# Performance work log

Measured on AMD Instinct MI355X. Metric: run time of the kernel, lower is better.

## Reference

```python
import jax, jax.numpy as jnp
import numpy as np

D = 32       # hidden_size (hardcoded in AR.__init__)
H = 16       # num_heads
HD = D // H  # head_dim = 2
L = 8        # num DiT blocks
MLP = 128    # mlp_ratio 4.0
B, S, T, P = 16, 1024, 256, 32
SCALE = float(1.0 / np.sqrt(HD))


def _ln(x, g, b, eps=1e-6):
    mu = jnp.mean(x, axis=-1, keepdims=True)
    var = jnp.mean((x - mu) ** 2, axis=-1, keepdims=True)
    return (x - mu) * jax.lax.rsqrt(var + eps) * g + b


def _mha(q_in, kv_in, in_w, in_b, out_w, out_b):
    # nn.MultiheadAttention math, batch-first layout (permutation-equivalent)
    wq, wk, wv = in_w[:D], in_w[D:2 * D], in_w[2 * D:]
    bq, bk, bv = in_b[:D], in_b[D:2 * D], in_b[2 * D:]
    Bq, Sq = q_in.shape[0], q_in.shape[1]
    Sk = kv_in.shape[1]
    q = (q_in @ wq.T + bq).reshape(Bq, Sq, H, HD)
    k = (kv_in @ wk.T + bk).reshape(Bq, Sk, H, HD)
    v = (kv_in @ wv.T + bv).reshape(Bq, Sk, H, HD)
    scores = jnp.einsum('bqhd,bkhd->bhqk', q, k) * SCALE
    a = jax.nn.softmax(scores, axis=-1)
    o = jnp.einsum('bhqk,bkhd->bqhd', a, v).reshape(Bq, Sq, D)
    return o @ out_w.T + out_b


def setup_inputs() -> dict:
    key = jax.random.key(0)
    ks = iter(jax.random.split(key, 40))
    rn = lambda k, sh, sc=1.0: jax.random.normal(k, sh, jnp.float32) * sc
    inp = {
        'x': rn(next(ks), (B, S, D)),
        'speaker_emb': rn(next(ks), (B, P, D)),
        'text_phonemes': rn(next(ks), (B, T, D)),
        'timestep_emb': rn(next(ks), (B, D)),
        'mask': jnp.ones((S,), jnp.float32),
        # per-block params, stacked over L for lax.scan
        'ln1_g': jnp.ones((L, D)), 'ln1_b': jnp.zeros((L, D)),
        'ln2_g': jnp.ones((L, D)), 'ln2_b': jnp.zeros((L, D)),
        'ln22_g': jnp.ones((L, D)), 'ln22_b': jnp.zeros((L, D)),
        'ln3_g': jnp.ones((L, D)), 'ln3_b': jnp.zeros((L, D)),
        'attn_in_w': rn(next(ks), (L, 3 * D, D), 0.1), 'attn_in_b': jnp.zeros((L, 3 * D)),
        'attn_out_w': rn(next(ks), (L, D, D), 0.1), 'attn_out_b': jnp.zeros((L, D)),
        'cross_in_w': rn(next(ks), (L, 3 * D, D), 0.1), 'cross_in_b': jnp.zeros((L, 3 * D)),
        'cross_out_w': rn(next(ks), (L, D, D), 0.1), 'cross_out_b': jnp.zeros((L, D)),
        'ts_w': rn(next(ks), (L, 2 * D, D), 0.1), 'ts_b': jnp.zeros((L, 2 * D)),
        'fc1_w': rn(next(ks), (L, MLP, D), 0.1), 'fc1_b': jnp.zeros((L, MLP)),
        'fc2_w': rn(next(ks), (L, D, MLP), 0.1), 'fc2_b': jnp.zeros((L, D)),
    }
    return inp


def _forward(x, speaker_emb, text_phonemes, timestep_emb, mask, params):
    m = mask[None, :, None]  # (1, S, 1), matches mask.unsqueeze(0).unsqueeze(2)
    def body(h, p):
        h = h * m
        hn = _ln(h, p['ln1_g'], p['ln1_b'])
        h = h + _mha(hn, hn, p['attn_in_w'], p['attn_in_b'], p['attn_out_w'], p['attn_out_b'])
        # both cross attentions use cross_attn weights (cross_attn2 is dead code in source)
        ca1 = _mha(_ln(h, p['ln2_g'], p['ln2_b']), text_phonemes,
                   p['cross_in_w'], p['cross_in_b'], p['cross_out_w'], p['cross_out_b'])
        ca2 = _mha(_ln(h, p['ln22_g'], p['ln22_b']), speaker_emb,
                   p['cross_in_w'], p['cross_in_b'], p['cross_out_w'], p['cross_out_b'])
        h = h + ca1 + ca2
        ss = timestep_emb @ p['ts_w'].T + p['ts_b']        # (B, 2D)
        scale, shift = ss[:, :D], ss[:, D:]
        hm = _ln(h, p['ln3_g'], p['ln3_b']) * (1.0 + scale[:, None, :]) + shift[:, None, :]
        mlp = jax.nn.gelu(hm @ p['fc1_w'].T + p['fc1_b'], approximate=False) @ p['fc2_w'].T + p['fc2_b']
        return (h + mlp) * m, None
    out, _ = jax.lax.scan(body, x, params)
    return out


def reference(x, speaker_emb, text_phonemes, timestep_emb, mask,
              ln1_g, ln1_b, ln2_g, ln2_b, ln22_g, ln22_b, ln3_g, ln3_b,
              attn_in_w, attn_in_b, attn_out_w, attn_out_b,
              cross_in_w, cross_in_b, cross_out_w, cross_out_b,
              ts_w, ts_b, fc1_w, fc1_b, fc2_w, fc2_b):
    params = dict(ln1_g=ln1_g, ln1_b=ln1_b, ln2_g=ln2_g, ln2_b=ln2_b,
                  ln22_g=ln22_g, ln22_b=ln22_b, ln3_g=ln3_g, ln3_b=ln3_b,
                  attn_in_w=attn_in_w, attn_in_b=attn_in_b,
                  attn_out_w=attn_out_w, attn_out_b=attn_out_b,
                  cross_in_w=cross_in_w, cross_in_b=cross_in_b,
                  cross_out_w=cross_out_w, cross_out_b=cross_out_b,
                  ts_w=ts_w, ts_b=ts_b, fc1_w=fc1_w, fc1_b=fc1_b,
                  fc2_w=fc2_w, fc2_b=fc2_b)
    return _forward(x, speaker_emb, text_phonemes, timestep_emb, mask, params)
```

## Files before the change

### kernel.cpp

```cpp
#include <hip/hip_runtime.h>
#include <math.h>

#define NB 16
#define SEQ 1024
#define NT 16384
#define TT 256
#define PP 32
#define NL 8
#define SCALE 0.70710678118654752f
#define LOG2E 1.4426950408889634f
#define CS (SCALE * LOG2E)

static __device__ __forceinline__ float exp2fast(float x) {
#if __has_builtin(__builtin_amdgcn_exp2f)
  return __builtin_amdgcn_exp2f(x);
#else
  return exp2f(x);
#endif
}

__global__ __launch_bounds__(256) void k_ss(const float* __restrict__ tse,
                                            const float* __restrict__ tsw,
                                            const float* __restrict__ tsb,
                                            float* __restrict__ out) {
  int idx = blockIdx.x * 256 + threadIdx.x;
  if (idx >= NL * NB * 64) return;
  int l = idx >> 10;
  int rem = idx & 1023;
  int b = rem >> 6;
  int j = rem & 63;
  const float* wr = tsw + ((size_t)l * 64 + j) * 32;
  const float* xr = tse + b * 32;
  float acc = tsb[l * 64 + j];
#pragma unroll
  for (int e = 0; e < 32; e++) acc = fmaf(xr[e], wr[e], acc);
  out[idx] = acc;
}

__global__ __launch_bounds__(256) void k_kv(const float* __restrict__ src,
                                            const float* __restrict__ wbase,
                                            const float* __restrict__ bbase,
                                            float* __restrict__ dstbase,
                                            int ntok) {
  __shared__ float sh[64 * 33];
  int tid = threadIdx.x;
  int l = blockIdx.y;
  int tok0 = blockIdx.x * 64;
  const float* w = wbase + (size_t)l * 96 * 32;
  const float* wb = bbase + (size_t)l * 96;
  float* dst = dstbase + (size_t)l * 64 * ntok;
  for (int i = tid; i < 64 * 32; i += 256) {
    int tl = i >> 5, e = i & 31;
    sh[tl * 33 + e] = src[(size_t)(tok0 + tl) * 32 + e];
  }
  __syncthreads();
  int tl = tid & 63;
  int wv = tid >> 6;
#pragma unroll
  for (int k = 0; k < 16; k++) {
    int j = __builtin_amdgcn_readfirstlane(wv + 4 * k);
    const float* wr = w + j * 32;
    const float* hr = sh + tl * 33;
    float acc = wb[j];
#pragma unroll
    for (int e = 0; e < 32; e++) acc = fmaf(hr[e], wr[e], acc);
    dst[(size_t)j * ntok + tok0 + tl] = acc;
  }
}

__device__ __forceinline__ void load_row32(const float* __restrict__ base, int tok, float* r) {
#pragma unroll
  for (int e = 0; e < 32; e++) r[e] = base[(size_t)e * NT + tok];
}

__device__ __forceinline__ void ln_core(float* r) {
  float a0 = 0, a1 = 0, a2 = 0, a3 = 0;
#pragma unroll
  for (int e = 0; e < 32; e += 4) { a0 += r[e]; a1 += r[e + 1]; a2 += r[e + 2]; a3 += r[e + 3]; }
  float mu = ((a0 + a1) + (a2 + a3)) * (1.0f / 32.0f);
  float v0 = 0, v1 = 0, v2 = 0, v3 = 0;
#pragma unroll
  for (int e = 0; e < 32; e += 4) {
    float d0 = r[e] - mu, d1 = r[e + 1] - mu, d2 = r[e + 2] - mu, d3 = r[e + 3] - mu;
    v0 = fmaf(d0, d0, v0); v1 = fmaf(d1, d1, v1); v2 = fmaf(d2, d2, v2); v3 = fmaf(d3, d3, v3);
  }
  float rstd = rsqrtf(((v0 + v1) + (v2 + v3)) * (1.0f / 32.0f) + 1e-6f);
#pragma unroll
  for (int e = 0; e < 32; e++) r[e] = (r[e] - mu) * rstd;
}

__global__ __launch_bounds__(256) void k_qkv(const float* __restrict__ hin,
                                             int rowmajor,
                                             float* __restrict__ hT,
                                             const float* __restrict__ mask,
                                             const float* __restrict__ w,
                                             const float* __restrict__ wb,
                                             const float* __restrict__ g,
                                             const float* __restrict__ bv,
                                             float* __restrict__ qkvT) {
  int tid = threadIdx.x;
  int tok0 = blockIdx.x * 64;
  int yc = blockIdx.y;
  int tl = tid & 63, wv = tid >> 6;
  int tok = tok0 + tl;
  float r[32];
  if (rowmajor) {
    float m = mask[tok & (SEQ - 1)];
#pragma unroll
    for (int e = 0; e < 32; e++) r[e] = hin[(size_t)tok * 32 + e] * m;
    if (yc == 0 && wv == 0) {
#pragma unroll
      for (int e = 0; e < 32; e++) hT[(size_t)e * NT + tok] = r[e];
    }
  } else {
    load_row32(hin, tok, r);
  }
  ln_core(r);
#pragma unroll
  for (int e = 0; e < 32; e++) r[e] = fmaf(r[e], g[e], bv[e]);
#pragma unroll
  for (int k = 0; k < 6; k++) {
    int j = __builtin_amdgcn_readfirstlane(yc * 24 + wv + 4 * k);
    const float* wr = w + j * 32;
    float acc = wb[j];
#pragma unroll
    for (int e = 0; e < 32; e++) acc = fmaf(r[e], wr[e], acc);
    qkvT[(size_t)j * NT + tok] = acc;
  }
}

__global__ __launch_bounds__(256) void k_q12(const float* __restrict__ hT,
                                             const float* __restrict__ w,
                                             const float* __restrict__ wb,
                                             const float* __restrict__ g2, const float* __restrict__ b2,
                                             const float* __restrict__ g22, const float* __restrict__ b22,
                                             float* __restrict__ q1T, float* __restrict__ q2T) {
  int tid = threadIdx.x;
  int tok0 = blockIdx.x * 64, yc = blockIdx.y;
  int tl = tid & 63, wv = tid >> 6;
  int tok = tok0 + tl;
  float r[32];
  load_row32(hT, tok, r);
  ln_core(r);
  const float* g = (yc >= 2) ? g22 : g2;
  const float* bb = (yc >= 2) ? b22 : b2;
  float* dst = (yc >= 2) ? q2T : q1T;
#pragma unroll
  for (int e = 0; e < 32; e++) r[e] = fmaf(r[e], g[e], bb[e]);
  int jbase = (yc & 1) * 16;
#pragma unroll
  for (int k = 0; k < 4; k++) {
    int j = __builtin_amdgcn_readfirstlane(jbase + wv + 4 * k);
    const float* wr = w + j * 32;
    float acc = wb[j];
#pragma unroll
    for (int e = 0; e < 32; e++) acc = fmaf(r[e], wr[e], acc);
    dst[(size_t)j * NT + tok] = acc;
  }
}

__global__ __launch_bounds__(256) void k_proj_add(const float* __restrict__ s1T,
                                                  const float* __restrict__ s2T,
                                                  const float* __restrict__ w,
                                                  const float* __restrict__ wb, float bmult,
                                                  float* __restrict__ hT) {
  int tid = threadIdx.x;
  int tok0 = blockIdx.x * 64, yc = blockIdx.y;
  int tl = tid & 63, wv = tid >> 6;
  int tok = tok0 + tl;
  float r[32];
  if (s2T) {
#pragma unroll
    for (int e = 0; e < 32; e++)
      r[e] = s1T[(size_t)e * NT + tok] + s2T[(size_t)e * NT + tok];
  } else {
    load_row32(s1T, tok, r);
  }
#pragma unroll
  for (int k = 0; k < 2; k++) {
    int j = __builtin_amdgcn_readfirstlane(yc * 8 + wv + 4 * k);
    const float* wr = w + j * 32;
    float acc = bmult * wb[j];
#pragma unroll
    for (int e = 0; e < 32; e++) acc = fmaf(r[e], wr[e], acc);
    size_t gi = (size_t)j * NT + tok;
    hT[gi] += acc;
  }
}

template <int SK>
__device__ __forceinline__ void attn_body(const float* __restrict__ qb,
                                          const float* __restrict__ kb,
                                          const float* __restrict__ vb,
                                          int kv_ld,
                                          float* __restrict__ ob,
                                          float2* kk, float2* vv, float* red) {
  int tid = threadIdx.x;
  int bx = blockIdx.x;
  int chunk = bx & 3, bh = bx >> 2;
  int b = bh >> 4, hh = bh & 15;
  const float* kxr = kb + (size_t)(2 * hh) * kv_ld + b * SK;
  const float* kyr = kxr + kv_ld;
  const float* vxr = vb + (size_t)(2 * hh) * kv_ld + b * SK;
  const float* vyr = vxr + kv_ld;
  float mx = 0.f, my = 0.f;
  for (int i = tid; i < SK; i += 256) {
    float kx = kxr[i], ky = kyr[i];
    kk[i] = make_float2(kx, ky);
    vv[i] = make_float2(vxr[i], vyr[i]);
    mx = fmaxf(mx, fabsf(kx));
    my = fmaxf(my, fabsf(ky));
  }
#pragma unroll
  for (int off = 32; off > 0; off >>= 1) {
    mx = fmaxf(mx, __shfl_xor(mx, off));
    my = fmaxf(my, __shfl_xor(my, off));
  }
  if ((tid & 63) == 0) { red[(tid >> 6) * 2] = mx; red[(tid >> 6) * 2 + 1] = my; }
  __syncthreads();
  mx = fmaxf(fmaxf(red[0], red[2]), fmaxf(red[4], red[6]));
  my = fmaxf(fmaxf(red[1], red[3]), fmaxf(red[5], red[7]));

  int r = chunk * 256 + tid;
  const float* qxr = qb + (size_t)(2 * hh) * NT + b * SEQ;
  const float* qyr = qxr + NT;
  float qx = qxr[r] * CS, qy = qyr[r] * CS;
  float mn = -(fabsf(qx) * mx + fabsf(qy) * my);
  float s0 = 0, s1 = 0, s2 = 0, s3 = 0;
  float ox0 = 0, ox1 = 0, ox2 = 0, ox3 = 0, oy0 = 0, oy1 = 0, oy2 = 0, oy3 = 0;
  for (int s = 0; s < SK; s += 4) {
    float2 ka = kk[s], kb2 = kk[s + 1], kc = kk[s + 2], kd = kk[s + 3];
    float2 va = vv[s], vb2 = vv[s + 1], vc = vv[s + 2], vd = vv[s + 3];
    float e0 = exp2fast(fmaf(qx, ka.x, fmaf(qy, ka.y, mn)));
    float e1 = exp2fast(fmaf(qx, kb2.x, fmaf(qy, kb2.y, mn)));
    float e2 = exp2fast(fmaf(qx, kc.x, fmaf(qy, kc.y, mn)));
    float e3 = exp2fast(fmaf(qx, kd.x, fmaf(qy, kd.y, mn)));
    s0 += e0; s1 += e1; s2 += e2; s3 += e3;
    ox0 = fmaf(e0, va.x, ox0); oy0 = fmaf(e0, va.y, oy0);
    ox1 = fmaf(e1, vb2.x, ox1); oy1 = fmaf(e1, vb2.y, oy1);
    ox2 = fmaf(e2, vc.x, ox2); oy2 = fmaf(e2, vc.y, oy2);
    ox3 = fmaf(e3, vd.x, ox3); oy3 = fmaf(e3, vd.y, oy3);
  }
  float sum = (s0 + s1) + (s2 + s3);
  float inv = 1.0f / sum;
  float* oxr = ob + (size_t)(2 * hh) * NT + b * SEQ;
  float* oyr = oxr + NT;
  oxr[r] = ((ox0 + ox1) + (ox2 + ox3)) * inv;
  oyr[r] = ((oy0 + oy1) + (oy2 + oy3)) * inv;
}

__global__ __launch_bounds__(256) void k_attn_self(const float* __restrict__ qkvT,
                                                   float* __restrict__ oT) {
  __shared__ float2 kk[1024], vv[1024];
  __shared__ float red[8];
  attn_body<SEQ>(qkvT, qkvT + (size_t)32 * NT, qkvT + (size_t)64 * NT, NT, oT, kk, vv, red);
}

__global__ __launch_bounds__(256) void k_attn_cross(const float* __restrict__ q1T,
                                                    const float* __restrict__ q2T,
                                                    const float* __restrict__ kvt,
                                                    const float* __restrict__ kvs,
                                                    float* __restrict__ o1T,
                                                    float* __restrict__ o2T) {
  __shared__ float2 kk[TT], vv[TT];
  __shared__ float red[8];
  if (blockIdx.y == 0)
    attn_body<TT>(q1T, kvt, kvt + (size_t)32 * (NB * TT), NB * TT, o1T, kk, vv, red);
  else
    attn_body<PP>(q2T, kvs, kvs + (size_t)32 * (NB * PP), NB * PP, o2T, kk, vv, red);
}

__global__ __launch_bounds__(256) void k_fc1(const float* __restrict__ hT,
                                             const float* __restrict__ ssl,
                                             const float* __restrict__ g, const float* __restrict__ bv,
                                             const float* __restrict__ w1, const float* __restrict__ b1,
                                             float* __restrict__ uT) {
  int tid = threadIdx.x;
  int tok0 = blockIdx.x * 64, yc = blockIdx.y;
  int tl = tid & 63, wv = tid >> 6;
  int tok = tok0 + tl;
  int b = tok0 >> 10;
  const float* sc = ssl + b * 64;
  float r[32];
  load_row32(hT, tok, r);
  ln_core(r);
#pragma unroll
  for (int e = 0; e < 32; e++) {
    float ln = fmaf(r[e], g[e], bv[e]);
    r[e] = fmaf(ln, 1.0f + sc[e], sc[32 + e]);
  }
#pragma unroll
  for (int k = 0; k < 8; k++) {
    int j = __builtin_amdgcn_readfirstlane(yc * 32 + wv + 4 * k);
    const float* wr = w1 + j * 32;
    float acc = b1[j];
#pragma unroll
    for (int e = 0; e < 32; e++) acc = fmaf(r[e], wr[e], acc);
    float ge = 0.5f * acc * (1.0f + erff(acc * 0.70710678118654752f));
    uT[(size_t)j * NT + tok] = ge;
  }
}

__global__ __launch_bounds__(256) void k_fc2(const float* __restrict__ uT,
                                             float* __restrict__ hT,
                                             float* __restrict__ out_rm,
                                             const float* __restrict__ mask,
                                             const float* __restrict__ w2,
                                             const float* __restrict__ b2) {
  __shared__ __align__(16) float shu[64 * 132];
  int tid = threadIdx.x;
  int tok0 = blockIdx.x * 64, yc = blockIdx.y;
  for (int i = tid; i < 64 * 128; i += 256) {
    int e = i >> 6, tl = i & 63;
    shu[tl * 132 + e] = uT[(size_t)e * NT + tok0 + tl];
  }
  __syncthreads();
  int tl = tid & 63, wv = tid >> 6;
  int tok = tok0 + tl;
  int j0 = __builtin_amdgcn_readfirstlane(yc * 16 + wv);
  int j1 = __builtin_amdgcn_readfirstlane(j0 + 4);
  int j2 = __builtin_amdgcn_readfirstlane(j0 + 8);
  int j3 = __builtin_amdgcn_readfirstlane(j0 + 12);
  const float* w0 = w2 + j0 * 128;
  const float* w1 = w2 + j1 * 128;
  const float* w2r = w2 + j2 * 128;
  const float* w3 = w2 + j3 * 128;
  float a0 = b2[j0], a1 = b2[j1], a2 = b2[j2], a3 = b2[j3];
  const float4* ur = (const float4*)(shu + tl * 132);
#pragma unroll
  for (int m = 0; m < 32; m++) {
    float4 t = ur[m];
    a0 = fmaf(t.x, w0[4 * m], a0); a0 = fmaf(t.y, w0[4 * m + 1], a0);
    a0 = fmaf(t.z, w0[4 * m + 2], a0); a0 = fmaf(t.w, w0[4 * m + 3], a0);
    a1 = fmaf(t.x, w1[4 * m], a1); a1 = fmaf(t.y, w1[4 * m + 1], a1);
    a1 = fmaf(t.z, w1[4 * m + 2], a1); a1 = fmaf(t.w, w1[4 * m + 3], a1);
    a2 = fmaf(t.x, w2r[4 * m], a2); a2 = fmaf(t.y, w2r[4 * m + 1], a2);
    a2 = fmaf(t.z, w2r[4 * m + 2], a2); a2 = fmaf(t.w, w2r[4 * m + 3], a2);
    a3 = fmaf(t.x, w3[4 * m], a3); a3 = fmaf(t.y, w3[4 * m + 1], a3);
    a3 = fmaf(t.z, w3[4 * m + 2], a3); a3 = fmaf(t.w, w3[4 * m + 3], a3);
  }
  float mk = mask[tok & (SEQ - 1)];
  float r0 = (hT[(size_t)j0 * NT + tok] + a0) * mk;
  float r1 = (hT[(size_t)j1 * NT + tok] + a1) * mk;
  float r2 = (hT[(size_t)j2 * NT + tok] + a2) * mk;
  float r3 = (hT[(size_t)j3 * NT + tok] + a3) * mk;
  if (out_rm) {
    out_rm[(size_t)tok * 32 + j0] = r0;
    out_rm[(size_t)tok * 32 + j1] = r1;
    out_rm[(size_t)tok * 32 + j2] = r2;
    out_rm[(size_t)tok * 32 + j3] = r3;
  } else {
    hT[(size_t)j0 * NT + tok] = r0;
    hT[(size_t)j1 * NT + tok] = r1;
    hT[(size_t)j2 * NT + tok] = r2;
    hT[(size_t)j3 * NT + tok] = r3;
  }
}

extern "C" void kernel_launch(void* const* d_in, const int* in_sizes, int n_in,
                              void* d_out, int out_size, void* d_ws, size_t ws_size,
                              hipStream_t stream) {
  const float* x = (const float*)d_in[0];
  const float* spk = (const float*)d_in[1];
  const float* text = (const float*)d_in[2];
  const float* tse = (const float*)d_in[3];
  const float* mask = (const float*)d_in[4];
  const float* ln1_g = (const float*)d_in[5];
  const float* ln1_b = (const float*)d_in[6];
  const float* ln2_g = (const float*)d_in[7];
  const float* ln2_b = (const float*)d_in[8];
  const float* ln22_g = (const float*)d_in[9];
  const float* ln22_b = (const float*)d_in[10];
  const float* ln3_g = (const float*)d_in[11];
  const float* ln3_b = (const float*)d_in[12];
  const float* aw = (const float*)d_in[13];
  const float* ab = (const float*)d_in[14];
  const float* aow = (const float*)d_in[15];
  const float* aob = (const float*)d_in[16];
  const float* cw = (const float*)d_in[17];
  const float* cb = (const float*)d_in[18];
  const float* cow = (const float*)d_in[19];
  const float* cob = (const float*)d_in[20];
  const float* tsw = (const float*)d_in[21];
  const float* tsb = (const float*)d_in[22];
  const float* f1w = (const float*)d_in[23];
  const float* f1b = (const float*)d_in[24];
  const float* f2w = (const float*)d_in[25];
  const float* f2b = (const float*)d_in[26];

  float* ws = (float*)d_ws;
  float* hT = ws;
  float* qkvT = hT + (size_t)32 * NT;
  float* o1T = qkvT + (size_t)96 * NT;
  float* o2T = o1T + (size_t)32 * NT;
  float* q1T = o2T + (size_t)32 * NT;
  float* q2T = q1T + (size_t)32 * NT;
  float* kvtT = q2T + (size_t)32 * NT;
  float* kvsT = kvtT + (size_t)NL * 64 * (NB * TT);
  float* ssa = kvsT + (size_t)NL * 64 * (NB * PP);
  float* uT = o1T;

  k_ss<<<32, 256, 0, stream>>>(tse, tsw, tsb, ssa);
  k_kv<<<dim3(64, NL), 256, 0, stream>>>(text, cw + 32 * 32, cb + 32, kvtT, NB * TT);
  k_kv<<<dim3(8, NL), 256, 0, stream>>>(spk, cw + 32 * 32, cb + 32, kvsT, NB * PP);

  for (int l = 0; l < NL; l++) {
    k_qkv<<<dim3(256, 4), 256, 0, stream>>>((l == 0) ? x : hT, (l == 0) ? 1 : 0, hT, mask,
                                            aw + (size_t)l * 96 * 32, ab + l * 96,
                                            ln1_g + l * 32, ln1_b + l * 32, qkvT);
    k_attn_self<<<1024, 256, 0, stream>>>(qkvT, o1T);
    k_proj_add<<<dim3(256, 4), 256, 0, stream>>>(o1T, nullptr,
                                                 aow + (size_t)l * 32 * 32, aob + l * 32, 1.0f, hT);
    k_q12<<<dim3(256, 4), 256, 0, stream>>>(hT, cw + (size_t)l * 96 * 32, cb + l * 96,
                                            ln2_g + l * 32, ln2_b + l * 32,
                                            ln22_g + l * 32, ln22_b + l * 32, q1T, q2T);
    k_attn_cross<<<dim3(1024, 2), 256, 0, stream>>>(q1T, q2T,
                                                    kvtT + (size_t)l * 64 * (NB * TT),
                                                    kvsT + (size_t)l * 64 * (NB * PP),
                                                    o1T, o2T);
    k_proj_add<<<dim3(256, 4), 256, 0, stream>>>(o1T, o2T,
                                                 cow + (size_t)l * 32 * 32, cob + l * 32, 2.0f, hT);
    k_fc1<<<dim3(256, 4), 256, 0, stream>>>(hT, ssa + (size_t)l * NB * 64,
                                            ln3_g + l * 32, ln3_b + l * 32,
                                            f1w + (size_t)l * 128 * 32, f1b + l * 128, uT);
    k_fc2<<<dim3(256, 2), 256, 0, stream>>>(uT, hT, (l == NL - 1) ? (float*)d_out : nullptr,
                                            mask, f2w + (size_t)l * 32 * 128, f2b + l * 32);
  }
}
```

Measured before the change: 964.3 us.

## Split attention keys across lane groups with packed FMA and fuse preprocessing kernels

The attention kernel is restructured so that each group of 16 lanes splits the key range for 4 queries. Keys and values are read directly from global memory as float4 instead of being staged in LDS, the score and accumulation math uses packed 2-wide float FMAs, and partial sums are combined with shuffles. The grid grows from 1024 to 4096 blocks per attention launch, and the block-wide max-magnitude pass is removed along with its barrier, so softmax no longer has an overflow safeguard. The timestep-modulation and cross-attention K/V precompute kernels are merged into a single launch to save launch overhead.

```diff
diff --git a/kernel.cpp b/kernel.cpp
--- a/kernel.cpp
+++ b/kernel.cpp
@@ -11,6 +11,8 @@
 #define LOG2E 1.4426950408889634f
 #define CS (SCALE * LOG2E)
 
+typedef float v2f __attribute__((ext_vector_type(2)));
+
 static __device__ __forceinline__ float exp2fast(float x) {
 #if __has_builtin(__builtin_amdgcn_exp2f)
   return __builtin_amdgcn_exp2f(x);
@@ -19,36 +21,45 @@
 #endif
 }
 
-__global__ __launch_bounds__(256) void k_ss(const float* __restrict__ tse,
-                                            const float* __restrict__ tsw,
-                                            const float* __restrict__ tsb,
-                                            float* __restrict__ out) {
-  int idx = blockIdx.x * 256 + threadIdx.x;
-  if (idx >= NL * NB * 64) return;
-  int l = idx >> 10;
-  int rem = idx & 1023;
-  int b = rem >> 6;
-  int j = rem & 63;
-  const float* wr = tsw + ((size_t)l * 64 + j) * 32;
-  const float* xr = tse + b * 32;
-  float acc = tsb[l * 64 + j];
-#pragma unroll
-  for (int e = 0; e < 32; e++) acc = fmaf(xr[e], wr[e], acc);
-  out[idx] = acc;
-}
-
-__global__ __launch_bounds__(256) void k_kv(const float* __restrict__ src,
-                                            const float* __restrict__ wbase,
-                                            const float* __restrict__ bbase,
-                                            float* __restrict__ dstbase,
-                                            int ntok) {
+__global__ __launch_bounds__(256) void k_pre(const float* __restrict__ tse,
+                                             const float* __restrict__ tsw,
+                                             const float* __restrict__ tsb,
+                                             float* __restrict__ ssa,
+                                             const float* __restrict__ text,
+                                             const float* __restrict__ spk,
+                                             const float* __restrict__ cw,
+                                             const float* __restrict__ cb,
+                                             float* __restrict__ kvtT,
+                                             float* __restrict__ kvsT) {
   __shared__ float sh[64 * 33];
   int tid = threadIdx.x;
-  int l = blockIdx.y;
-  int tok0 = blockIdx.x * 64;
-  const float* w = wbase + (size_t)l * 96 * 32;
-  const float* wb = bbase + (size_t)l * 96;
-  float* dst = dstbase + (size_t)l * 64 * ntok;
+  int bx = blockIdx.x;
+  if (bx < 32) {
+    int idx = bx * 256 + tid;
+    int l = idx >> 10;
+    int rem = idx & 1023;
+    int b = rem >> 6;
+    int j = rem & 63;
+    const float* wr = tsw + ((size_t)l * 64 + j) * 32;
+    const float* xr = tse + b * 32;
+    float acc = tsb[l * 64 + j];
+#pragma unroll
+    for (int e = 0; e < 32; e++) acc = fmaf(xr[e], wr[e], acc);
+    ssa[idx] = acc;
+    return;
+  }
+  const float* src;
+  float* dst;
+  int l, tok0, ntok;
+  if (bx < 544) {
+    l = (bx - 32) >> 6; tok0 = ((bx - 32) & 63) * 64; ntok = NB * TT; src = text;
+    dst = kvtT + (size_t)l * 64 * ntok;
+  } else {
+    l = (bx - 544) >> 3; tok0 = ((bx - 544) & 7) * 64; ntok = NB * PP; src = spk;
+    dst = kvsT + (size_t)l * 64 * ntok;
+  }
+  const float* w = cw + (size_t)l * 96 * 32 + 32 * 32;
+  const float* wb = cb + (size_t)l * 96 + 32;
   for (int i = tid; i < 64 * 32; i += 256) {
     int tl = i >> 5, e = i & 31;
     sh[tl * 33 + e] = src[(size_t)(tok0 + tl) * 32 + e];
@@ -189,71 +200,102 @@
 }
 
 template <int SK>
-__device__ __forceinline__ void attn_body(const float* __restrict__ qb,
+__device__ __forceinline__ void attn_core(const float* __restrict__ qb,
                                           const float* __restrict__ kb,
                                           const float* __restrict__ vb,
-                                          int kv_ld,
-                                          float* __restrict__ ob,
-                                          float2* kk, float2* vv, float* red) {
+                                          int kvld,
+                                          float* __restrict__ ob) {
   int tid = threadIdx.x;
   int bx = blockIdx.x;
-  int chunk = bx & 3, bh = bx >> 2;
+  int rc = bx & 15, bh = bx >> 4;
   int b = bh >> 4, hh = bh & 15;
-  const float* kxr = kb + (size_t)(2 * hh) * kv_ld + b * SK;
-  const float* kyr = kxr + kv_ld;
-  const float* vxr = vb + (size_t)(2 * hh) * kv_ld + b * SK;
-  const float* vyr = vxr + kv_ld;
-  float mx = 0.f, my = 0.f;
-  for (int i = tid; i < SK; i += 256) {
-    float kx = kxr[i], ky = kyr[i];
-    kk[i] = make_float2(kx, ky);
-    vv[i] = make_float2(vxr[i], vyr[i]);
-    mx = fmaxf(mx, fabsf(kx));
-    my = fmaxf(my, fabsf(ky));
-  }
-#pragma unroll
-  for (int off = 32; off > 0; off >>= 1) {
-    mx = fmaxf(mx, __shfl_xor(mx, off));
-    my = fmaxf(my, __shfl_xor(my, off));
-  }
-  if ((tid & 63) == 0) { red[(tid >> 6) * 2] = mx; red[(tid >> 6) * 2 + 1] = my; }
-  __syncthreads();
-  mx = fmaxf(fmaxf(red[0], red[2]), fmaxf(red[4], red[6]));
-  my = fmaxf(fmaxf(red[1], red[3]), fmaxf(red[5], red[7]));
-
-  int r = chunk * 256 + tid;
-  const float* qxr = qb + (size_t)(2 * hh) * NT + b * SEQ;
-  const float* qyr = qxr + NT;
-  float qx = qxr[r] * CS, qy = qyr[r] * CS;
-  float mn = -(fabsf(qx) * mx + fabsf(qy) * my);
-  float s0 = 0, s1 = 0, s2 = 0, s3 = 0;
-  float ox0 = 0, ox1 = 0, ox2 = 0, ox3 = 0, oy0 = 0, oy1 = 0, oy2 = 0, oy3 = 0;
-  for (int s = 0; s < SK; s += 4) {
-    float2 ka = kk[s], kb2 = kk[s + 1], kc = kk[s + 2], kd = kk[s + 3];
-    float2 va = vv[s], vb2 = vv[s + 1], vc = vv[s + 2], vd = vv[s + 3];
-    float e0 = exp2fast(fmaf(qx, ka.x, fmaf(qy, ka.y, mn)));
-    float e1 = exp2fast(fmaf(qx, kb2.x, fmaf(qy, kb2.y, mn)));
-    float e2 = exp2fast(fmaf(qx, kc.x, fmaf(qy, kc.y, mn)));
-    float e3 = exp2fast(fmaf(qx, kd.x, fmaf(qy, kd.y, mn)));
-    s0 += e0; s1 += e1; s2 += e2; s3 += e3;
-    ox0 = fmaf(e0, va.x, ox0); oy0 = fmaf(e0, va.y, oy0);
-    ox1 = fmaf(e1, vb2.x, ox1); oy1 = fmaf(e1, vb2.y, oy1);
-    ox2 = fmaf(e2, vc.x, ox2); oy2 = fmaf(e2, vc.y, oy2);
-    ox3 = fmaf(e3, vd.x, ox3); oy3 = fmaf(e3, vd.y, oy3);
-  }
-  float sum = (s0 + s1) + (s2 + s3);
-  float inv = 1.0f / sum;
-  float* oxr = ob + (size_t)(2 * hh) * NT + b * SEQ;
-  float* oyr = oxr + NT;
-  oxr[r] = ((ox0 + ox1) + (ox2 + ox3)) * inv;
-  oyr[r] = ((oy0 + oy1) + (oy2 + oy3)) * inv;
+  int wv = tid >> 6, lane = tid & 63;
+  int rg = lane >> 4, kl = lane & 15;
+  int rbase = rc * 64 + wv * 16 + rg;
+
+  const float* qx = qb + (size_t)(2 * hh) * NT + b * SEQ;
+  const float* qy = qx + NT;
+  const float* kx = kb + (size_t)(2 * hh) * kvld + b * SK;
+  const float* ky = kx + kvld;
+  const float* vx = vb + (size_t)(2 * hh) * kvld + b * SK;
+  const float* vy = vx + kvld;
+
+  v2f qxx[4], qyy[4], sum2[4], ox2[4], oy2[4];
+#pragma unroll
+  for (int s = 0; s < 4; s++) {
+    float q1 = qx[rbase + 4 * s] * CS;
+    float q2 = qy[rbase + 4 * s] * CS;
+    qxx[s] = (v2f){q1, q1};
+    qyy[s] = (v2f){q2, q2};
+    sum2[s] = (v2f){0.f, 0.f};
+    ox2[s] = (v2f){0.f, 0.f};
+    oy2[s] = (v2f){0.f, 0.f};
+  }
+
+  if constexpr (SK >= 64) {
+#pragma unroll 2
+    for (int c = 0; c < SK / 64; c++) {
+      int o = c * 64 + kl * 4;
+      float4 kx4 = *(const float4*)(kx + o);
+      float4 ky4 = *(const float4*)(ky + o);
+      float4 vx4 = *(const float4*)(vx + o);
+      float4 vy4 = *(const float4*)(vy + o);
+      v2f kxlo = (v2f){kx4.x, kx4.y}, kxhi = (v2f){kx4.z, kx4.w};
+      v2f kylo = (v2f){ky4.x, ky4.y}, kyhi = (v2f){ky4.z, ky4.w};
+      v2f vxlo = (v2f){vx4.x, vx4.y}, vxhi = (v2f){vx4.z, vx4.w};
+      v2f vylo = (v2f){vy4.x, vy4.y}, vyhi = (v2f){vy4.z, vy4.w};
+#pragma unroll
+      for (int s = 0; s < 4; s++) {
+        v2f tlo = __builtin_elementwise_fma(qyy[s], kylo, qxx[s] * kxlo);
+        v2f thi = __builtin_elementwise_fma(qyy[s], kyhi, qxx[s] * kxhi);
+        v2f elo = (v2f){exp2fast(tlo[0]), exp2fast(tlo[1])};
+        v2f ehi = (v2f){exp2fast(thi[0]), exp2fast(thi[1])};
+        sum2[s] += elo;
+        sum2[s] += ehi;
+        ox2[s] = __builtin_elementwise_fma(elo, vxlo, ox2[s]);
+        ox2[s] = __builtin_elementwise_fma(ehi, vxhi, ox2[s]);
+        oy2[s] = __builtin_elementwise_fma(elo, vylo, oy2[s]);
+        oy2[s] = __builtin_elementwise_fma(ehi, vyhi, oy2[s]);
+      }
+    }
+  } else {
+    v2f kx2 = *(const v2f*)(kx + kl * 2);
+    v2f ky2 = *(const v2f*)(ky + kl * 2);
+    v2f vx2 = *(const v2f*)(vx + kl * 2);
+    v2f vy2 = *(const v2f*)(vy + kl * 2);
+#pragma unroll
+    for (int s = 0; s < 4; s++) {
+      v2f t = __builtin_elementwise_fma(qyy[s], ky2, qxx[s] * kx2);
+      v2f e = (v2f){exp2fast(t[0]), exp2fast(t[1])};
+      sum2[s] += e;
+      ox2[s] = __builtin_elementwise_fma(e, vx2, ox2[s]);
+      oy2[s] = __builtin_elementwise_fma(e, vy2, oy2[s]);
+    }
+  }
+
+#pragma unroll
+  for (int s = 0; s < 4; s++) {
+    float sm = sum2[s][0] + sum2[s][1];
+    float ox = ox2[s][0] + ox2[s][1];
+    float oy = oy2[s][0] + oy2[s][1];
+#pragma unroll
+    for (int off = 1; off < 16; off <<= 1) {
+      sm += __shfl_xor(sm, off);
+      ox += __shfl_xor(ox, off);
+      oy += __shfl_xor(oy, off);
+    }
+    if (kl == 0) {
+      float inv = 1.0f / sm;
+      int tok = b * SEQ + rbase + 4 * s;
+      ob[(size_t)(2 * hh) * NT + tok] = ox * inv;
+      ob[(size_t)(2 * hh + 1) * NT + tok] = oy * inv;
+    }
+  }
 }
 
 __global__ __launch_bounds__(256) void k_attn_self(const float* __restrict__ qkvT,
                                                    float* __restrict__ oT) {
-  __shared__ float2 kk[1024], vv[1024];
-  __shared__ float red[8];
-  attn_body<SEQ>(qkvT, qkvT + (size_t)32 * NT, qkvT + (size_t)64 * NT, NT, oT, kk, vv, red);
+  attn_core<SEQ>(qkvT, qkvT + (size_t)32 * NT, qkvT + (size_t)64 * NT, NT, oT);
 }
 
 __global__ __launch_bounds__(256) void k_attn_cross(const float* __restrict__ q1T,
@@ -262,12 +304,10 @@
                                                     const float* __restrict__ kvs,
                                                     float* __restrict__ o1T,
                                                     float* __restrict__ o2T) {
-  __shared__ float2 kk[TT], vv[TT];
-  __shared__ float red[8];
   if (blockIdx.y == 0)
-    attn_body<TT>(q1T, kvt, kvt + (size_t)32 * (NB * TT), NB * TT, o1T, kk, vv, red);
+    attn_core<TT>(q1T, kvt, kvt + (size_t)32 * (NB * TT), NB * TT, o1T);
   else
-    attn_body<PP>(q2T, kvs, kvs + (size_t)32 * (NB * PP), NB * PP, o2T, kk, vv, red);
+    attn_core<PP>(q2T, kvs, kvs + (size_t)32 * (NB * PP), NB * PP, o2T);
 }
 
 __global__ __launch_bounds__(256) void k_fc1(const float* __restrict__ hT,
@@ -400,21 +440,19 @@
   float* ssa = kvsT + (size_t)NL * 64 * (NB * PP);
   float* uT = o1T;
 
-  k_ss<<<32, 256, 0, stream>>>(tse, tsw, tsb, ssa);
-  k_kv<<<dim3(64, NL), 256, 0, stream>>>(text, cw + 32 * 32, cb + 32, kvtT, NB * TT);
-  k_kv<<<dim3(8, NL), 256, 0, stream>>>(spk, cw + 32 * 32, cb + 32, kvsT, NB * PP);
+  k_pre<<<608, 256, 0, stream>>>(tse, tsw, tsb, ssa, text, spk, cw, cb, kvtT, kvsT);
 
   for (int l = 0; l < NL; l++) {
     k_qkv<<<dim3(256, 4), 256, 0, stream>>>((l == 0) ? x : hT, (l == 0) ? 1 : 0, hT, mask,
                                             aw + (size_t)l * 96 * 32, ab + l * 96,
                                             ln1_g + l * 32, ln1_b + l * 32, qkvT);
-    k_attn_self<<<1024, 256, 0, stream>>>(qkvT, o1T);
+    k_attn_self<<<4096, 256, 0, stream>>>(qkvT, o1T);
     k_proj_add<<<dim3(256, 4), 256, 0, stream>>>(o1T, nullptr,
                                                  aow + (size_t)l * 32 * 32, aob + l * 32, 1.0f, hT);
     k_q12<<<dim3(256, 4), 256, 0, stream>>>(hT, cw + (size_t)l * 96 * 32, cb + l * 96,
                                             ln2_g + l * 32, ln2_b + l * 32,
                                             ln22_g + l * 32, ln22_b + l * 32, q1T, q2T);
-    k_attn_cross<<<dim3(1024, 2), 256, 0, stream>>>(q1T, q2T,
+    k_attn_cross<<<dim3(4096, 2), 256, 0, stream>>>(q1T, q2T,
                                                     kvtT + (size_t)l * 64 * (NB * TT),
                                                     kvsT + (size_t)l * 64 * (NB * PP),
                                                     o1T, o2T);
```

Measured after the change: 915.3 us. 1.05x faster.
